# Optimization experiments

Hardware: AMD Instinct MI355X
Metric: run time of the kernel (lower is better)

The kernel has to match this reference:

```python
import jax, jax.numpy as jnp
from jax import lax
import numpy as np

B, S, D, H, L, DFF = 64, 512, 512, 8, 6, 2048
CLIP_C = 10.0
EPS = 1e-5


def setup_inputs() -> dict:
    key = jax.random.key(0)
    ks = jax.random.split(key, 16)
    sc = 0.02
    inp = {
        "x": jax.random.normal(ks[0], (B, S, D), jnp.float32),
        "mask": jnp.zeros((B, S, S), jnp.float32),
        # stacked per-layer params [L, ...]; Linear stored as (out, in) like torch
        "qkv_w": jax.random.normal(ks[1], (L, 3 * D, D), jnp.float32) * sc,
        "qkv_b": jnp.zeros((L, 3 * D), jnp.float32),
        "ln1_g": jnp.ones((L, D), jnp.float32),
        "ln1_b": jnp.zeros((L, D), jnp.float32),
        "kv_w": jax.random.normal(ks[2], (L, 2 * D, D), jnp.float32) * sc,
        "kv_b": jnp.zeros((L, 2 * D), jnp.float32),
        "ln2_g": jnp.ones((L, D), jnp.float32),
        "ln2_b": jnp.zeros((L, D), jnp.float32),
        "w1": jax.random.normal(ks[3], (L, DFF, D), jnp.float32) * sc,
        "b1": jnp.zeros((L, DFF), jnp.float32),
        "w2": jax.random.normal(ks[4], (L, D, DFF), jnp.float32) * sc,
        "b2": jnp.zeros((L, D), jnp.float32),
        "ln3_g": jnp.ones((L, D), jnp.float32),
        "ln3_b": jnp.zeros((L, D), jnp.float32),
    }
    return inp


def _ln(v, g, b):
    m = v.mean(-1, keepdims=True)
    var = ((v - m) ** 2).mean(-1, keepdims=True)
    return (v - m) * lax.rsqrt(var + EPS) * g + b


def _mha(q, k, v, mask, clip_c):
    # faithful to custom_multi_head_attn: bmm -> /sqrt(hd) -> [c*tanh] -> +mask -> softmax -> bmm
    b, sq, d = q.shape
    sk = k.shape[1]
    hd = d // H
    qh = q.reshape(b, sq, H, hd)
    kh = k.reshape(b, sk, H, hd)
    vh = v.reshape(b, sk, H, hd)
    s = jnp.einsum('bqhd,bkhd->bhqk', qh, kh) * (1.0 / float(hd) ** 0.5)
    if clip_c is not None:
        s = clip_c * jnp.tanh(s)
    if mask is not None:
        s = s + mask[:, None]  # repeat over heads
    a = jax.nn.softmax(s, axis=-1)
    return jnp.einsum('bhqk,bkhd->bqhd', a, vh).reshape(b, sq, d)


def reference(x, mask, qkv_w, qkv_b, ln1_g, ln1_b, kv_w, kv_b, ln2_g, ln2_b,
              w1, b1, w2, b2, ln3_g, ln3_b):
    def step(h, p):
        (qw, qb, g1, be1, kw, kb, g2, be2, fw1, fb1, fw2, fb2, g3, be3) = p
        # self-attention block (no FFN, no mask, no clip; note: NO out-projection,
        # matching the original which never applies out_proj_weight)
        qkv = h @ qw.T + qb
        q, k, v = jnp.split(qkv, 3, axis=-1)
        x1 = _ln(h + _mha(q, k, v, None, None), g1, be1)
        # cross-attention block: query = sa output (no q_proj), kv from original h
        kv_ = h @ kw.T + kb
        k2, v2 = jnp.split(kv_, 2, axis=-1)
        y = _ln(x1 + _mha(x1, k2, v2, mask, CLIP_C), g2, be2)
        # FFN + residual + norm (post-norm)
        ff = jax.nn.relu(y @ fw1.T + fb1) @ fw2.T + fb2
        return _ln(y + ff, g3, be3), None

    params = (qkv_w, qkv_b, ln1_g, ln1_b, kv_w, kv_b, ln2_g, ln2_b,
              w1, b1, w2, b2, ln3_g, ln3_b)
    out, _ = lax.scan(step, x, params)
    return out
```

## Files before the change

kernel.cpp:

```cpp
#include <hip/hip_runtime.h>


typedef __bf16 bf16_t;
typedef __bf16 bf16x8 __attribute__((ext_vector_type(8)));
typedef __bf16 bf16x4 __attribute__((ext_vector_type(4)));
typedef float  f32x4  __attribute__((ext_vector_type(4)));

#define NB   64
#define NS   512
#define ND   512
#define NH   8
#define NHD  64
#define NL   6
#define NDFF 2048
#define NM   (NB * NS)

__device__ __forceinline__ void gld_lds16(const void* gsrc, void* lds) {
  __builtin_amdgcn_global_load_lds((__attribute__((address_space(1))) void*)gsrc,
                                   (__attribute__((address_space(3))) void*)lds,
                                   16, 0, 0);
}

template<int N> __device__ __forceinline__ void vm_wait() {
  if constexpr (N == 0)      asm volatile("s_waitcnt vmcnt(0)" ::: "memory");
  else if constexpr (N == 8) asm volatile("s_waitcnt vmcnt(8)" ::: "memory");
}
__device__ __forceinline__ void lgkm0() {
  asm volatile("s_waitcnt lgkmcnt(0)" ::: "memory");
}

__global__ __launch_bounds__(256) void cvt_f32_bf16(const float* __restrict__ in,
                                                    bf16_t* __restrict__ out,
                                                    long n) {
  long i = ((long)blockIdx.x * 256 + threadIdx.x) * 8;
  const long stride = (long)gridDim.x * 256 * 8;
  for (; i < n; i += stride) {
    f32x4 a = *(const f32x4*)(in + i);
    f32x4 b = *(const f32x4*)(in + i + 4);
    bf16x8 o;
#pragma unroll
    for (int j = 0; j < 4; ++j) { o[j] = (bf16_t)a[j]; o[j + 4] = (bf16_t)b[j]; }
    *(bf16x8*)(out + i) = o;
  }
}

template<bool RELU, bool BIAS_ROW>
__global__ __launch_bounds__(256) void gemm97(const bf16_t* __restrict__ Ap,
                                              const bf16_t* __restrict__ Wp,
                                              const float* __restrict__ bias,
                                              bf16_t* __restrict__ Cout,
                                              int Nn, int Kk) {
  __shared__ __attribute__((aligned(16))) bf16_t As[2][128 * 64];
  __shared__ __attribute__((aligned(16))) bf16_t Bs[2][128 * 64];
  const int tid = threadIdx.x;
  const int l   = tid & 63;
  const int w   = tid >> 6;
  const int wr  = (w >> 1) * 64;
  const int wc  = (w & 1) * 64;
  const int l15 = l & 15, lg = l >> 4;

  const int nn   = Nn >> 7;
  const int nwg  = gridDim.x;
  const int flat = blockIdx.x;
  const int wgid = (nwg & 7) ? flat : (flat & 7) * (nwg >> 3) + (flat >> 3);
  const int m0 = (wgid / nn) * 128;
  const int n0 = (wgid % nn) * 128;

  const int prow = w * 32 + (l >> 3);

  auto stage = [&](int kt, int bf_) {
    const int kc = kt * 64;
#pragma unroll
    for (int i = 0; i < 4; ++i) {
      const int rA = prow + i * 8;
      const int g  = (l & 7) ^ (rA & 7);
      gld_lds16(Ap + (size_t)(m0 + rA) * Kk + kc + g * 8, &As[bf_][(w * 4 + i) * 512]);
    }
#pragma unroll
    for (int i = 0; i < 4; ++i) {
      const int rB = prow + i * 8;
      const int g  = (l & 7) ^ (rB & 7);
      gld_lds16(Wp + (size_t)(n0 + rB) * Kk + kc + g * 8, &Bs[bf_][(w * 4 + i) * 512]);
    }
  };
  auto ldA = [&](int bf_, int mi, int kk) -> bf16x8 {
    const int row = wr + mi * 16 + l15;
    return *(const bf16x8*)&As[bf_][row * 64 + (((kk * 4 + lg) ^ (row & 7)) * 8)];
  };
  auto ldB = [&](int bf_, int ni, int kk) -> bf16x8 {
    const int row = wc + ni * 16 + l15;
    return *(const bf16x8*)&Bs[bf_][row * 64 + (((kk * 4 + lg) ^ (row & 7)) * 8)];
  };

  f32x4 acc[4][4];
#pragma unroll
  for (int i = 0; i < 4; ++i)
#pragma unroll
    for (int j = 0; j < 4; ++j) acc[i][j] = (f32x4){0.f, 0.f, 0.f, 0.f};

  const int KT = Kk >> 6;
  stage(0, 0);

  int buf = 0;
  for (int kt = 0; kt < KT; ++kt) {
    if (kt + 1 < KT) { stage(kt + 1, buf ^ 1); vm_wait<8>(); }
    else             vm_wait<0>();
    __builtin_amdgcn_s_barrier();
#pragma unroll
    for (int kk = 0; kk < 2; ++kk) {
      bf16x8 af[4], bw[4];
#pragma unroll
      for (int i = 0; i < 4; ++i) { af[i] = ldA(buf, i, kk); bw[i] = ldB(buf, i, kk); }
      __builtin_amdgcn_s_setprio(1);
#pragma unroll
      for (int mi = 0; mi < 4; ++mi)
#pragma unroll
        for (int ni = 0; ni < 4; ++ni)
          acc[mi][ni] = __builtin_amdgcn_mfma_f32_16x16x32_bf16(af[mi], bw[ni], acc[mi][ni], 0, 0, 0);
      __builtin_amdgcn_s_setprio(0);
    }
    lgkm0();
    __builtin_amdgcn_s_barrier();
    buf ^= 1;
  }

#pragma unroll
  for (int mi = 0; mi < 4; ++mi)
#pragma unroll
    for (int ni = 0; ni < 4; ++ni) {
      const int col = n0 + wc + ni * 16 + l15;
      const float bc = BIAS_ROW ? 0.f : bias[col];
#pragma unroll
      for (int r = 0; r < 4; ++r) {
        const int rowi = m0 + wr + mi * 16 + lg * 4 + r;
        float v = acc[mi][ni][r] + (BIAS_ROW ? bias[rowi] : bc);
        if (RELU) v = fmaxf(v, 0.f);
        Cout[(size_t)rowi * Nn + col] = (bf16_t)v;
      }
    }
}

template<int CROSS, bool M16>
__global__ __launch_bounds__(256, 2) void attn5(const bf16_t* __restrict__ Q,
                                                const bf16_t* __restrict__ K,
                                                const bf16_t* __restrict__ Vt,
                                                const void* __restrict__ maskp,
                                                bf16_t* __restrict__ O,
                                                int qstride, int kstride, int vstride) {
  __shared__ __attribute__((aligned(16))) bf16_t k_s[2][64 * 64];
  __shared__ __attribute__((aligned(16))) bf16_t v_s[2][64 * 64];
  __shared__ __attribute__((aligned(16))) bf16_t p_s[64 * 64];

  const int tid = threadIdx.x;
  const int l   = tid & 63;
  const int w   = tid >> 6;
  const int bid = blockIdx.x;
  const int h   = bid & 7;
  const int qt  = (bid >> 3) & 7;
  const int b   = bid >> 6;
  const int h64 = h * NHD;
  const int l15 = l & 15, lg = l >> 4;

  const int qglob = qt * 64 + w * 16 + l15;

  auto stageK = [&](int kt, int buf) {
#pragma unroll
    for (int i = 0; i < 2; ++i) {
      const int r  = i * 32 + (tid >> 3);
      const int c8 = (tid & 7) ^ (r & 7);
      gld_lds16(K + (size_t)(b * NS + kt * 64 + r) * kstride + h64 + c8 * 8,
                &k_s[buf][(i * 32 + w * 8) * 64]);
    }
  };
  auto stageV = [&](int kt, int buf) {
#pragma unroll
    for (int i = 0; i < 2; ++i) {
      const int d = i * 32 + (tid >> 3);
      const int g = (tid & 7) ^ (d & 7);
      gld_lds16(Vt + (size_t)(h64 + d) * vstride + b * NS + kt * 64 + g * 8,
                &v_s[buf][(i * 32 + w * 8) * 64]);
    }
  };

  stageK(0, 0); stageV(0, 0);

  bf16x8 qf[2];
#pragma unroll
  for (int c = 0; c < 2; ++c)
    qf[c] = *(const bf16x8*)(Q + (size_t)(b * NS + qglob) * qstride + h64 + c * 32 + lg * 8);

  bf16x4 mk16[2][4];
  f32x4  mkf[2][4];
  if (CROSS) {
#pragma unroll
    for (int nt = 0; nt < 4; ++nt) {
      if (M16) mk16[0][nt] = *(const bf16x4*)((const bf16_t*)maskp
                              + (size_t)(b * NS + qglob) * NS + nt * 16 + lg * 4);
      else     mkf[0][nt]  = *(const f32x4*)((const float*)maskp
                              + (size_t)(b * NS + qglob) * NS + nt * 16 + lg * 4);
    }
  }

  float m_run = -3e38f, l_run = 0.f;
  const f32x4 zz = {0.f, 0.f, 0.f, 0.f};
  f32x4 oacc[4] = {zz, zz, zz, zz};

#pragma unroll
  for (int kt = 0; kt < 8; ++kt) {
    const int buf = kt & 1;
    __syncthreads();
    if (kt < 7) {
      stageK(kt + 1, buf ^ 1);
      stageV(kt + 1, buf ^ 1);
      if (CROSS) {
#pragma unroll
        for (int nt = 0; nt < 4; ++nt) {
          if (M16) mk16[buf ^ 1][nt] = *(const bf16x4*)((const bf16_t*)maskp
                     + (size_t)(b * NS + qglob) * NS + (kt + 1) * 64 + nt * 16 + lg * 4);
          else     mkf[buf ^ 1][nt]  = *(const f32x4*)((const float*)maskp
                     + (size_t)(b * NS + qglob) * NS + (kt + 1) * 64 + nt * 16 + lg * 4);
        }
      }
    }

    f32x4 s[4];
    __builtin_amdgcn_s_setprio(1);
#pragma unroll
    for (int nt = 0; nt < 4; ++nt) {
      const int row = nt * 16 + l15;
      bf16x8 ka0 = *(const bf16x8*)((const char*)k_s[buf] + row * 128 + ((lg ^ (row & 7)) * 16));
      bf16x8 ka1 = *(const bf16x8*)((const char*)k_s[buf] + row * 128 + (((4 + lg) ^ (row & 7)) * 16));
      f32x4 z = zz;
      z = __builtin_amdgcn_mfma_f32_16x16x32_bf16(ka0, qf[0], z, 0, 0, 0);
      z = __builtin_amdgcn_mfma_f32_16x16x32_bf16(ka1, qf[1], z, 0, 0, 0);
      s[nt] = z;
    }
    __builtin_amdgcn_s_setprio(0);

    float tmax = -3e38f;
#pragma unroll
    for (int nt = 0; nt < 4; ++nt) {
      f32x4 v = s[nt] * 0.125f;
      if (CROSS) {
#pragma unroll
        for (int r = 0; r < 4; ++r) {
          const float e2 = __expf(2.f * v[r]);
          const float mkv = M16 ? (float)mk16[buf][nt][r] : mkf[buf][nt][r];
          v[r] = 10.f - 20.f * __builtin_amdgcn_rcpf(e2 + 1.f) + mkv;
        }
      }
      s[nt] = v;
#pragma unroll
      for (int r = 0; r < 4; ++r) tmax = fmaxf(tmax, v[r]);
    }
    tmax = fmaxf(tmax, __shfl_xor(tmax, 16, 64));
    tmax = fmaxf(tmax, __shfl_xor(tmax, 32, 64));
    const float m_new = fmaxf(m_run, tmax);
    const float f = __expf(m_run - m_new);
    float fq[4];
#pragma unroll
    for (int r = 0; r < 4; ++r) fq[r] = __shfl(f, lg * 4 + r, 64);
#pragma unroll
    for (int dt = 0; dt < 4; ++dt)
#pragma unroll
      for (int r = 0; r < 4; ++r) oacc[dt][r] *= fq[r];

    float ts = 0.f;
#pragma unroll
    for (int nt = 0; nt < 4; ++nt) {
      f32x4 v = s[nt];
#pragma unroll
      for (int r = 0; r < 4; ++r) { const float e = __expf(v[r] - m_new); ts += e; v[r] = e; }
      s[nt] = v;
    }
    l_run = l_run * f + ts;
    m_run = m_new;

    const int prow = w * 16 + l15;
#pragma unroll
    for (int nt = 0; nt < 4; ++nt) {
      bf16x4 pk;
#pragma unroll
      for (int r = 0; r < 4; ++r) pk[r] = (bf16_t)s[nt][r];
      const int gran = (nt * 2 + (lg >> 1)) ^ (prow & 7);
      *(bf16x4*)((char*)p_s + prow * 128 + gran * 16 + (lg & 1) * 8) = pk;
    }

    __builtin_amdgcn_s_setprio(1);
#pragma unroll
    for (int ks = 0; ks < 2; ++ks) {
      const int ag = (ks * 4 + lg) ^ (prow & 7);
      bf16x8 pa = *(const bf16x8*)((const char*)p_s + prow * 128 + ag * 16);
#pragma unroll
      for (int dt = 0; dt < 4; ++dt) {
        const int vrow = dt * 16 + l15;
        const int vg   = (ks * 4 + lg) ^ (vrow & 7);
        bf16x8 vb = *(const bf16x8*)((const char*)v_s[buf] + vrow * 128 + vg * 16);
        oacc[dt] = __builtin_amdgcn_mfma_f32_16x16x32_bf16(pa, vb, oacc[dt], 0, 0, 0);
      }
    }
    __builtin_amdgcn_s_setprio(0);
  }

  l_run += __shfl_xor(l_run, 16, 64);
  l_run += __shfl_xor(l_run, 32, 64);
  const float inv = 1.f / l_run;
  float invq[4];
#pragma unroll
  for (int r = 0; r < 4; ++r) invq[r] = __shfl(inv, lg * 4 + r, 64);
#pragma unroll
  for (int dt = 0; dt < 4; ++dt)
#pragma unroll
    for (int r = 0; r < 4; ++r) {
      const size_t row = (size_t)(b * NS + qt * 64 + w * 16 + lg * 4 + r);
      O[row * ND + h64 + dt * 16 + l15] = (bf16_t)(oacc[dt][r] * invq[r]);
    }
}

template<bool A16, bool W32>
__global__ __launch_bounds__(256) void add_ln2(const void* __restrict__ Xav,
                                               const bf16_t* __restrict__ Xb,
                                               const float* __restrict__ gw,
                                               const float* __restrict__ bw,
                                               float* __restrict__ o32,
                                               bf16_t* __restrict__ o16) {
  const int l = threadIdx.x & 63;
  const size_t row  = (size_t)blockIdx.x * 4 + (threadIdx.x >> 6);
  const size_t base = row * ND + l * 8;
  f32x4 a0, a1;
  if (A16) {
    bf16x8 t = *(const bf16x8*)((const bf16_t*)Xav + base);
#pragma unroll
    for (int i = 0; i < 4; ++i) { a0[i] = (float)t[i]; a1[i] = (float)t[i + 4]; }
  } else {
    a0 = *(const f32x4*)((const float*)Xav + base);
    a1 = *(const f32x4*)((const float*)Xav + base + 4);
  }
  bf16x8 tb = *(const bf16x8*)(Xb + base);
  f32x4 b0, b1;
#pragma unroll
  for (int i = 0; i < 4; ++i) { b0[i] = (float)tb[i]; b1[i] = (float)tb[i + 4]; }
  f32x4 v0 = a0 + b0, v1 = a1 + b1;
  float s = v0[0] + v0[1] + v0[2] + v0[3] + v1[0] + v1[1] + v1[2] + v1[3];
#pragma unroll
  for (int off = 1; off < 64; off <<= 1) s += __shfl_xor(s, off, 64);
  const float mean = s * (1.f / ND);
  f32x4 d0 = v0 - mean, d1 = v1 - mean;
  float q = d0[0]*d0[0] + d0[1]*d0[1] + d0[2]*d0[2] + d0[3]*d0[3]
          + d1[0]*d1[0] + d1[1]*d1[1] + d1[2]*d1[2] + d1[3]*d1[3];
#pragma unroll
  for (int off = 1; off < 64; off <<= 1) q += __shfl_xor(q, off, 64);
  const float rstd = rsqrtf(q * (1.f / ND) + 1e-5f);
  const f32x4 g0 = *(const f32x4*)(gw + l * 8), g1 = *(const f32x4*)(gw + l * 8 + 4);
  const f32x4 h0 = *(const f32x4*)(bw + l * 8), h1 = *(const f32x4*)(bw + l * 8 + 4);
  f32x4 r0 = d0 * rstd * g0 + h0;
  f32x4 r1 = d1 * rstd * g1 + h1;
  if (W32) {
    *(f32x4*)(o32 + base)     = r0;
    *(f32x4*)(o32 + base + 4) = r1;
  } else {
    bf16x8 o;
#pragma unroll
    for (int i = 0; i < 4; ++i) { o[i] = (bf16_t)r0[i]; o[i + 4] = (bf16_t)r1[i]; }
    *(bf16x8*)(o16 + base) = o;
  }
}

extern "C" void kernel_launch(void* const* d_in, const int* in_sizes, int n_in,
                              void* d_out, int out_size, void* d_ws, size_t ws_size,
                              hipStream_t stream) {
  (void)in_sizes; (void)n_in; (void)out_size;
  const float* x     = (const float*)d_in[0];
  const float* maskp = (const float*)d_in[1];
  const float* qkvw  = (const float*)d_in[2];
  const float* qkvb  = (const float*)d_in[3];
  const float* ln1g  = (const float*)d_in[4];
  const float* ln1b  = (const float*)d_in[5];
  const float* kvw   = (const float*)d_in[6];
  const float* kvb   = (const float*)d_in[7];
  const float* ln2g  = (const float*)d_in[8];
  const float* ln2b  = (const float*)d_in[9];
  const float* w1p   = (const float*)d_in[10];
  const float* b1p   = (const float*)d_in[11];
  const float* w2p   = (const float*)d_in[12];
  const float* b2p   = (const float*)d_in[13];
  const float* ln3g  = (const float*)d_in[14];
  const float* ln3b  = (const float*)d_in[15];
  float* out = (float*)d_out;

  const size_t WALL = 40894464, WLYR = 6815744, H16B = 33554432, M16B = 33554432;
  struct Tier { int R; bool allw; };
  const Tier tiers[6] = {{32768, true}, {16384, true}, {8192, true},
                         {4096, true}, {2048, false}, {1024, false}};
  int R = 0; bool allw = false; size_t base_need = 0;
  for (int t = 0; t < 6; ++t) {
    size_t need = (tiers[t].allw ? WALL : WLYR) + H16B +
                  (size_t)tiers[t].R * 7168 + 16384;
    if (ws_size >= need) { R = tiers[t].R; allw = tiers[t].allw; base_need = need; break; }
  }
  if (R == 0) return;
  const bool m16 = (ws_size >= base_need + M16B + 256);
  const int nchunks = NM / R;
  const int CB = R / NS;
  const int MT = R / 128;

  char* p = (char*)d_ws;
  auto alloc = [&](size_t bytes) { char* r = p; p += (bytes + 255) & ~(size_t)255; return r; };
  bf16_t* WQ = (bf16_t*)alloc((allw ? NL : 1) * (size_t)1536 * ND * 2);
  bf16_t* WK = (bf16_t*)alloc((allw ? NL : 1) * (size_t)1024 * ND * 2);
  bf16_t* W1 = (bf16_t*)alloc((allw ? NL : 1) * (size_t)NDFF * ND * 2);
  bf16_t* W2 = (bf16_t*)alloc((allw ? NL : 1) * (size_t)ND * NDFF * 2);
  bf16_t* h16  = (bf16_t*)alloc((size_t)NM * ND * 2);
  bf16_t* big  = (bf16_t*)alloc((size_t)R * NDFF * 2);
  bf16_t* t16  = (bf16_t*)alloc((size_t)R * ND * 2);
  bf16_t* x116 = (bf16_t*)alloc((size_t)R * ND * 2);
  bf16_t* y16  = (bf16_t*)alloc((size_t)R * ND * 2);
  bf16_t* mask16 = m16 ? (bf16_t*)alloc(M16B) : nullptr;

  auto cvt = [&](const float* src, bf16_t* dst, long n) {
    int blocks = (int)((n / 8 + 255) / 256); if (blocks > 8192) blocks = 8192;
    hipLaunchKernelGGL(cvt_f32_bf16, dim3(blocks), dim3(256), 0, stream, src, dst, n);
  };

  cvt(x, h16, (long)NM * ND);
  if (m16) cvt(maskp, mask16, (long)NM * NS);
  if (allw) {
    cvt(qkvw, WQ, (long)NL * 1536 * ND);
    cvt(kvw,  WK, (long)NL * 1024 * ND);
    cvt(w1p,  W1, (long)NL * NDFF * ND);
    cvt(w2p,  W2, (long)NL * ND * NDFF);
  }

  for (int l = 0; l < NL; ++l) {
    const bf16_t *wq_l, *wk_l, *w1_l, *w2_l;
    if (allw) {
      wq_l = WQ + (size_t)l * 1536 * ND;
      wk_l = WK + (size_t)l * 1024 * ND;
      w1_l = W1 + (size_t)l * NDFF * ND;
      w2_l = W2 + (size_t)l * ND * NDFF;
    } else {
      cvt(qkvw + (size_t)l * 1536 * ND, WQ, (long)1536 * ND);
      cvt(kvw  + (size_t)l * 1024 * ND, WK, (long)1024 * ND);
      cvt(w1p  + (size_t)l * NDFF * ND, W1, (long)NDFF * ND);
      cvt(w2p  + (size_t)l * ND * NDFF, W2, (long)ND * NDFF);
      wq_l = WQ; wk_l = WK; w1_l = W1; w2_l = W2;
    }

    for (int c = 0; c < nchunks; ++c) {
      const size_t r0 = (size_t)c * R;
      bf16_t*       h16c  = h16 + r0 * ND;
      bf16_t* vtS = big + (size_t)R * 1024;
      bf16_t* vtC = big + (size_t)R * 512;

      hipLaunchKernelGGL(HIP_KERNEL_NAME(gemm97<false, false>), dim3(MT * 8), dim3(256), 0, stream,
                         h16c, wq_l, qkvb + l * 1536, big, 1024, 512);
      hipLaunchKernelGGL(HIP_KERNEL_NAME(gemm97<false, true>), dim3(MT * 4), dim3(256), 0, stream,
                         wq_l + (size_t)1024 * 512, h16c, qkvb + l * 1536 + 1024, vtS, R, 512);
      hipLaunchKernelGGL(HIP_KERNEL_NAME(attn5<0, false>), dim3(CB * 64), dim3(256), 0, stream,
                         big, big + 512, vtS, (const void*)nullptr, t16, 1024, 1024, R);
      if (l == 0)
        hipLaunchKernelGGL(HIP_KERNEL_NAME(add_ln2<false, false>), dim3(R / 4), dim3(256), 0, stream,
                           (const void*)(x + r0 * ND), t16, ln1g, ln1b, (float*)nullptr, x116);
      else
        hipLaunchKernelGGL(HIP_KERNEL_NAME(add_ln2<true, false>), dim3(R / 4), dim3(256), 0, stream,
                           (const void*)h16c, t16, ln1g + l * ND, ln1b + l * ND, (float*)nullptr, x116);
      hipLaunchKernelGGL(HIP_KERNEL_NAME(gemm97<false, false>), dim3(MT * 4), dim3(256), 0, stream,
                         h16c, wk_l, kvb + l * 1024, big, 512, 512);
      hipLaunchKernelGGL(HIP_KERNEL_NAME(gemm97<false, true>), dim3(MT * 4), dim3(256), 0, stream,
                         wk_l + (size_t)512 * 512, h16c, kvb + l * 1024 + 512, vtC, R, 512);
      if (m16)
        hipLaunchKernelGGL(HIP_KERNEL_NAME(attn5<1, true>), dim3(CB * 64), dim3(256), 0, stream,
                           x116, big, vtC, (const void*)(mask16 + r0 * NS), t16, 512, 512, R);
      else
        hipLaunchKernelGGL(HIP_KERNEL_NAME(attn5<1, false>), dim3(CB * 64), dim3(256), 0, stream,
                           x116, big, vtC, (const void*)(maskp + r0 * NS), t16, 512, 512, R);
      hipLaunchKernelGGL(HIP_KERNEL_NAME(add_ln2<true, false>), dim3(R / 4), dim3(256), 0, stream,
                         (const void*)x116, t16, ln2g + l * ND, ln2b + l * ND, (float*)nullptr, y16);
      hipLaunchKernelGGL(HIP_KERNEL_NAME(gemm97<true, false>), dim3(MT * 16), dim3(256), 0, stream,
                         y16, w1_l, b1p + l * NDFF, big, 2048, 512);
      hipLaunchKernelGGL(HIP_KERNEL_NAME(gemm97<false, false>), dim3(MT * 4), dim3(256), 0, stream,
                         big, w2_l, b2p + l * ND, t16, 512, 2048);
      if (l < NL - 1)
        hipLaunchKernelGGL(HIP_KERNEL_NAME(add_ln2<true, false>), dim3(R / 4), dim3(256), 0, stream,
                           (const void*)y16, t16, ln3g + l * ND, ln3b + l * ND, (float*)nullptr, h16c);
      else
        hipLaunchKernelGGL(HIP_KERNEL_NAME(add_ln2<true, true>), dim3(R / 4), dim3(256), 0, stream,
                           (const void*)y16, t16, ln3g + l * ND, ln3b + l * ND, out + r0 * ND, (bf16_t*)nullptr);
    }
  }
}
```

Before: 3.812 ms.

## Make GEMM persistent with cross-tile prefetch of the next tile's first K-slice

Converts the GEMM kernel into a persistent variant where each workgroup processes several consecutive 128x128 output tiles, with the grid capped at 512 workgroups. While finishing the last K-step of one tile, it stages the first K-slice of the next tile, so load latency overlaps with the tail compute and epilogue. This is meant to cut workgroup launch and ramp-up overhead and hide pipeline bubbles between tiles. It assumes the tile count divides evenly by the grid and that the grid size is a multiple of 8. Giving each workgroup consecutive tiles may also change L2 reuse.

```diff
diff --git a/kernel.cpp b/kernel.cpp
--- a/kernel.cpp
+++ b/kernel.cpp
@@ -45,11 +45,11 @@
 }
 
 template<bool RELU, bool BIAS_ROW>
-__global__ __launch_bounds__(256) void gemm97(const bf16_t* __restrict__ Ap,
-                                              const bf16_t* __restrict__ Wp,
-                                              const float* __restrict__ bias,
-                                              bf16_t* __restrict__ Cout,
-                                              int Nn, int Kk) {
+__global__ __launch_bounds__(256) void gemm97p(const bf16_t* __restrict__ Ap,
+                                               const bf16_t* __restrict__ Wp,
+                                               const float* __restrict__ bias,
+                                               bf16_t* __restrict__ Cout,
+                                               int Nn, int Kk, int tpw) {
   __shared__ __attribute__((aligned(16))) bf16_t As[2][128 * 64];
   __shared__ __attribute__((aligned(16))) bf16_t Bs[2][128 * 64];
   const int tid = threadIdx.x;
@@ -62,25 +62,24 @@
   const int nn   = Nn >> 7;
   const int nwg  = gridDim.x;
   const int flat = blockIdx.x;
-  const int wgid = (nwg & 7) ? flat : (flat & 7) * (nwg >> 3) + (flat >> 3);
-  const int m0 = (wgid / nn) * 128;
-  const int n0 = (wgid % nn) * 128;
-
-  const int prow = w * 32 + (l >> 3);
-
-  auto stage = [&](int kt, int bf_) {
+  const int wgid = (flat & 7) * (nwg >> 3) + (flat >> 3);
+  const int tile0 = wgid * tpw;
+
+  const int srow = w * 32 + (l >> 3);
+
+  auto stage = [&](int mm, int nb, int kt, int bf_) {
     const int kc = kt * 64;
 #pragma unroll
     for (int i = 0; i < 4; ++i) {
-      const int rA = prow + i * 8;
+      const int rA = srow + i * 8;
       const int g  = (l & 7) ^ (rA & 7);
-      gld_lds16(Ap + (size_t)(m0 + rA) * Kk + kc + g * 8, &As[bf_][(w * 4 + i) * 512]);
+      gld_lds16(Ap + (size_t)(mm + rA) * Kk + kc + g * 8, &As[bf_][(w * 4 + i) * 512]);
     }
 #pragma unroll
     for (int i = 0; i < 4; ++i) {
-      const int rB = prow + i * 8;
+      const int rB = srow + i * 8;
       const int g  = (l & 7) ^ (rB & 7);
-      gld_lds16(Wp + (size_t)(n0 + rB) * Kk + kc + g * 8, &Bs[bf_][(w * 4 + i) * 512]);
+      gld_lds16(Wp + (size_t)(nb + rB) * Kk + kc + g * 8, &Bs[bf_][(w * 4 + i) * 512]);
     }
   };
   auto ldA = [&](int bf_, int mi, int kk) -> bf16x8 {
@@ -92,52 +91,62 @@
     return *(const bf16x8*)&Bs[bf_][row * 64 + (((kk * 4 + lg) ^ (row & 7)) * 8)];
   };
 
-  f32x4 acc[4][4];
-#pragma unroll
-  for (int i = 0; i < 4; ++i)
-#pragma unroll
-    for (int j = 0; j < 4; ++j) acc[i][j] = (f32x4){0.f, 0.f, 0.f, 0.f};
-
   const int KT = Kk >> 6;
-  stage(0, 0);
+  int m0 = (tile0 / nn) * 128;
+  int n0 = (tile0 % nn) * 128;
+  stage(m0, n0, 0, 0);
 
   int buf = 0;
-  for (int kt = 0; kt < KT; ++kt) {
-    if (kt + 1 < KT) { stage(kt + 1, buf ^ 1); vm_wait<8>(); }
-    else             vm_wait<0>();
-    __builtin_amdgcn_s_barrier();
-#pragma unroll
-    for (int kk = 0; kk < 2; ++kk) {
-      bf16x8 af[4], bw[4];
-#pragma unroll
-      for (int i = 0; i < 4; ++i) { af[i] = ldA(buf, i, kk); bw[i] = ldB(buf, i, kk); }
-      __builtin_amdgcn_s_setprio(1);
-#pragma unroll
-      for (int mi = 0; mi < 4; ++mi)
-#pragma unroll
-        for (int ni = 0; ni < 4; ++ni)
-          acc[mi][ni] = __builtin_amdgcn_mfma_f32_16x16x32_bf16(af[mi], bw[ni], acc[mi][ni], 0, 0, 0);
-      __builtin_amdgcn_s_setprio(0);
-    }
-    lgkm0();
-    __builtin_amdgcn_s_barrier();
-    buf ^= 1;
-  }
-
-#pragma unroll
-  for (int mi = 0; mi < 4; ++mi)
-#pragma unroll
-    for (int ni = 0; ni < 4; ++ni) {
-      const int col = n0 + wc + ni * 16 + l15;
-      const float bc = BIAS_ROW ? 0.f : bias[col];
-#pragma unroll
-      for (int r = 0; r < 4; ++r) {
-        const int rowi = m0 + wr + mi * 16 + lg * 4 + r;
-        float v = acc[mi][ni][r] + (BIAS_ROW ? bias[rowi] : bc);
-        if (RELU) v = fmaxf(v, 0.f);
-        Cout[(size_t)rowi * Nn + col] = (bf16_t)v;
+  for (int t = 0; t < tpw; ++t) {
+    const bool more = (t + 1 < tpw);
+    int m1 = 0, n1 = 0;
+    if (more) { const int nt_ = tile0 + t + 1; m1 = (nt_ / nn) * 128; n1 = (nt_ % nn) * 128; }
+
+    f32x4 acc[4][4];
+#pragma unroll
+    for (int i = 0; i < 4; ++i)
+#pragma unroll
+      for (int j = 0; j < 4; ++j) acc[i][j] = (f32x4){0.f, 0.f, 0.f, 0.f};
+
+    for (int kt = 0; kt < KT; ++kt) {
+      if (kt + 1 < KT)      { stage(m0, n0, kt + 1, buf ^ 1); vm_wait<8>(); }
+      else if (more)        { stage(m1, n1, 0, buf ^ 1);      vm_wait<8>(); }
+      else                  vm_wait<0>();
+      __builtin_amdgcn_s_barrier();
+#pragma unroll
+      for (int kk = 0; kk < 2; ++kk) {
+        bf16x8 af[4], bw[4];
+#pragma unroll
+        for (int i = 0; i < 4; ++i) { af[i] = ldA(buf, i, kk); bw[i] = ldB(buf, i, kk); }
+        __builtin_amdgcn_s_setprio(1);
+#pragma unroll
+        for (int mi = 0; mi < 4; ++mi)
+#pragma unroll
+          for (int ni = 0; ni < 4; ++ni)
+            acc[mi][ni] = __builtin_amdgcn_mfma_f32_16x16x32_bf16(af[mi], bw[ni], acc[mi][ni], 0, 0, 0);
+        __builtin_amdgcn_s_setprio(0);
       }
-    }
+      lgkm0();
+      __builtin_amdgcn_s_barrier();
+      buf ^= 1;
+    }
+
+#pragma unroll
+    for (int mi = 0; mi < 4; ++mi)
+#pragma unroll
+      for (int ni = 0; ni < 4; ++ni) {
+        const int col = n0 + wc + ni * 16 + l15;
+        const float bc = BIAS_ROW ? 0.f : bias[col];
+#pragma unroll
+        for (int r = 0; r < 4; ++r) {
+          const int rowi = m0 + wr + mi * 16 + lg * 4 + r;
+          float v = acc[mi][ni][r] + (BIAS_ROW ? bias[rowi] : bc);
+          if (RELU) v = fmaxf(v, 0.f);
+          Cout[(size_t)rowi * Nn + col] = (bf16_t)v;
+        }
+      }
+    m0 = m1; n0 = n1;
+  }
 }
 
 template<int CROSS, bool M16>
@@ -422,6 +431,9 @@
     hipLaunchKernelGGL(cvt_f32_bf16, dim3(blocks), dim3(256), 0, stream, src, dst, n);
   };
 
+  auto gtiles = [&](int M_, int N_) { return (M_ / 128) * (N_ / 128); };
+  auto ggrid  = [&](int tiles)      { return tiles > 512 ? 512 : tiles; };
+
   cvt(x, h16, (long)NM * ND);
   if (m16) cvt(maskp, mask16, (long)NM * NS);
   if (allw) {
@@ -452,10 +464,12 @@
       bf16_t* vtS = big + (size_t)R * 1024;
       bf16_t* vtC = big + (size_t)R * 512;
 
-      hipLaunchKernelGGL(HIP_KERNEL_NAME(gemm97<false, false>), dim3(MT * 8), dim3(256), 0, stream,
-                         h16c, wq_l, qkvb + l * 1536, big, 1024, 512);
-      hipLaunchKernelGGL(HIP_KERNEL_NAME(gemm97<false, true>), dim3(MT * 4), dim3(256), 0, stream,
-                         wq_l + (size_t)1024 * 512, h16c, qkvb + l * 1536 + 1024, vtS, R, 512);
+      { int tl = gtiles(R, 1024), g = ggrid(tl);
+        hipLaunchKernelGGL(HIP_KERNEL_NAME(gemm97p<false, false>), dim3(g), dim3(256), 0, stream,
+                           h16c, wq_l, qkvb + l * 1536, big, 1024, 512, tl / g); }
+      { int tl = gtiles(512, R), g = ggrid(tl);
+        hipLaunchKernelGGL(HIP_KERNEL_NAME(gemm97p<false, true>), dim3(g), dim3(256), 0, stream,
+                           wq_l + (size_t)1024 * 512, h16c, qkvb + l * 1536 + 1024, vtS, R, 512, tl / g); }
       hipLaunchKernelGGL(HIP_KERNEL_NAME(attn5<0, false>), dim3(CB * 64), dim3(256), 0, stream,
                          big, big + 512, vtS, (const void*)nullptr, t16, 1024, 1024, R);
       if (l == 0)
@@ -464,10 +478,12 @@
       else
         hipLaunchKernelGGL(HIP_KERNEL_NAME(add_ln2<true, false>), dim3(R / 4), dim3(256), 0, stream,
                            (const void*)h16c, t16, ln1g + l * ND, ln1b + l * ND, (float*)nullptr, x116);
-      hipLaunchKernelGGL(HIP_KERNEL_NAME(gemm97<false, false>), dim3(MT * 4), dim3(256), 0, stream,
-                         h16c, wk_l, kvb + l * 1024, big, 512, 512);
-      hipLaunchKernelGGL(HIP_KERNEL_NAME(gemm97<false, true>), dim3(MT * 4), dim3(256), 0, stream,
-                         wk_l + (size_t)512 * 512, h16c, kvb + l * 1024 + 512, vtC, R, 512);
+      { int tl = gtiles(R, 512), g = ggrid(tl);
+        hipLaunchKernelGGL(HIP_KERNEL_NAME(gemm97p<false, false>), dim3(g), dim3(256), 0, stream,
+                           h16c, wk_l, kvb + l * 1024, big, 512, 512, tl / g); }
+      { int tl = gtiles(512, R), g = ggrid(tl);
+        hipLaunchKernelGGL(HIP_KERNEL_NAME(gemm97p<false, true>), dim3(g), dim3(256), 0, stream,
+                           wk_l + (size_t)512 * 512, h16c, kvb + l * 1024 + 512, vtC, R, 512, tl / g); }
       if (m16)
         hipLaunchKernelGGL(HIP_KERNEL_NAME(attn5<1, true>), dim3(CB * 64), dim3(256), 0, stream,
                            x116, big, vtC, (const void*)(mask16 + r0 * NS), t16, 512, 512, R);
@@ -476,10 +492,12 @@
                            x116, big, vtC, (const void*)(maskp + r0 * NS), t16, 512, 512, R);
       hipLaunchKernelGGL(HIP_KERNEL_NAME(add_ln2<true, false>), dim3(R / 4), dim3(256), 0, stream,
                          (const void*)x116, t16, ln2g + l * ND, ln2b + l * ND, (float*)nullptr, y16);
-      hipLaunchKernelGGL(HIP_KERNEL_NAME(gemm97<true, false>), dim3(MT * 16), dim3(256), 0, stream,
-                         y16, w1_l, b1p + l * NDFF, big, 2048, 512);
-      hipLaunchKernelGGL(HIP_KERNEL_NAME(gemm97<false, false>), dim3(MT * 4), dim3(256), 0, stream,
-                         big, w2_l, b2p + l * ND, t16, 512, 2048);
+      { int tl = gtiles(R, 2048), g = ggrid(tl);
+        hipLaunchKernelGGL(HIP_KERNEL_NAME(gemm97p<true, false>), dim3(g), dim3(256), 0, stream,
+                           y16, w1_l, b1p + l * NDFF, big, 2048, 512, tl / g); }
+      { int tl = gtiles(R, 512), g = ggrid(tl);
+        hipLaunchKernelGGL(HIP_KERNEL_NAME(gemm97p<false, false>), dim3(g), dim3(256), 0, stream,
+                           big, w2_l, b2p + l * ND, t16, 512, 2048, tl / g); }
       if (l < NL - 1)
         hipLaunchKernelGGL(HIP_KERNEL_NAME(add_ln2<true, false>), dim3(R / 4), dim3(256), 0, stream,
                            (const void*)y16, t16, ln3g + l * ND, ln3b + l * ND, (float*)nullptr, h16c);
```

Result: no change. 3.868 ms (+1.5%).
